# Performance work log

Hardware: AMD Instinct MI355X
Metric: run time of the kernel (lower is better)

## Reference

```python
import jax, jax.numpy as jnp
import numpy as np

UNITS = 128
INPUT_DIM = 784
OUTPUT_DIM = 10
NUM_LAYERS = 8
BATCH = 2048
DT = 0.1
EPS = 0.01
TOL = 1e-4
STEPS = 15


def setup_inputs() -> dict:
    key = jax.random.key(0)
    k = jax.random.split(key, 7)
    s_in = 1.0 / np.sqrt(INPUT_DIM)
    s_u = 1.0 / np.sqrt(UNITS)
    return {
        "x": jax.random.normal(k[0], (BATCH, INPUT_DIM), jnp.float32),
        "w_in": jax.random.uniform(k[1], (UNITS, INPUT_DIM), jnp.float32, -s_in, s_in),
        "b_in": jax.random.uniform(k[2], (UNITS,), jnp.float32, -s_in, s_in),
        "w_blocks": jax.random.uniform(k[3], (NUM_LAYERS, UNITS, UNITS), jnp.float32, -s_u, s_u),
        "b_blocks": jax.random.uniform(k[4], (NUM_LAYERS, UNITS), jnp.float32, -s_u, s_u),
        "w_out": jax.random.uniform(k[5], (OUTPUT_DIM, UNITS), jnp.float32, -s_u, s_u),
        "b_out": jax.random.uniform(k[6], (OUTPUT_DIM,), jnp.float32, -s_u, s_u),
    }


def _build_A(w_blocks):
    # A_l = [[I, dt*W_l], [-dt*W_l^T, (1+dt/eps)*I]], shape [L, 2u, 2u]
    I = jnp.broadcast_to(jnp.eye(UNITS, dtype=w_blocks.dtype), (NUM_LAYERS, UNITS, UNITS))
    top = jnp.concatenate([I, DT * w_blocks], axis=2)
    bot = jnp.concatenate([-DT * jnp.transpose(w_blocks, (0, 2, 1)), (1.0 + DT / EPS) * I], axis=2)
    return jnp.concatenate([top, bot], axis=1)


def _sweep(z_in, A, b_blocks):
    # Fixed-point sweeping (no-grad region in the original). z_ls: [L, B, 2u]
    B = z_in.shape[0]

    def layer_step(z, xs):
        A_l, b_l, z_l = xs
        rhs = jnp.concatenate(
            [jnp.broadcast_to(DT * b_l, (B, UNITS)), (DT / EPS) * jnp.tanh(z_l[:, :UNITS])],
            axis=1,
        ) + z
        # A_l is shared across the batch: one LU, many rhs
        y = jnp.linalg.solve(A_l, rhs.T).T
        err = jnp.mean(jnp.linalg.norm(z_l - y, axis=1))
        return y, (y, err)

    def body(state):
        z_ls, _, step = state
        _, (new_zls, errs) = jax.lax.scan(layer_step, z_in, (A, b_blocks, z_ls))
        return (new_zls, jnp.mean(errs), step + 1)

    def cond(state):
        _, err, step = state
        return jnp.logical_and(step < STEPS, err > TOL)

    z0 = jnp.broadcast_to(z_in[None], (NUM_LAYERS,) + z_in.shape)
    z_ls, _, _ = jax.lax.while_loop(cond, body, (z0, jnp.float32(10.0), jnp.int32(0)))
    return z_ls


def _block(z_in, W, b, z_l):
    # implicit_forward of one TransNetLayerSweeping (z_l is the converged sweep state)
    u_l, v_l = z_l[:, :UNITS], z_l[:, UNITS:]
    u_out = -DT * (v_l @ W.T) + z_in[:, :UNITS] + DT * b
    v_out = DT * (u_l @ W) + z_in[:, UNITS:] - (DT / EPS) * (v_l - jnp.tanh(u_l))
    return jnp.concatenate([u_out, v_out], axis=1)


def reference(x, w_in, b_in, w_blocks, b_blocks, w_out, b_out):
    x1 = x @ w_in.T + b_in                                  # [B, u]
    z_in = jnp.concatenate([x1, jnp.tanh(x1)], axis=1)      # [B, 2u]
    z_ls = _sweep(z_in, _build_A(w_blocks), b_blocks)       # [L, B, 2u]
    # Original loop does z = block.implicit_forward(z_in) for every block,
    # so only the LAST block's output survives.
    z_out = _block(z_in, w_blocks[-1], b_blocks[-1], z_ls[-1])
    logits = z_out[:, :UNITS] @ w_out.T + b_out             # [B, out]
    return jax.nn.softmax(logits, axis=1)
```

## Files before the change

### kernel.cpp

```cpp
#include <hip/hip_runtime.h>

#define U 128
#define BATCH 2048
#define NL 8
#define NS 8
#define DTc 0.1f
#define TENf 10.0f
#define INVC (1.0f/11.0f)
#define AFACT (0.01f/11.0f)
#define AST 264
#define HST 136

typedef unsigned short u16;
typedef unsigned int u32;
typedef __attribute__((ext_vector_type(8))) short bf16x8;
typedef __attribute__((ext_vector_type(4))) float f32x4;
#define MFMA16(a,b,c) __builtin_amdgcn_mfma_f32_16x16x32_bf16(a,b,c,0,0,0)

#define SWZ8(row, c8)  (((row)<<7) + ((((c8) ^ ((row)&7)))<<3))
#define SWZE(row, col) (SWZ8(row, (col)>>3) + ((col)&7))

__device__ __forceinline__ float bf2f(u16 h){ return __uint_as_float(((u32)h)<<16); }
__device__ __forceinline__ u16 f2bf(float f){
  u32 u = __float_as_uint(f);
  u += 0x7FFFu + ((u >> 16) & 1u);
  return (u16)(u >> 16);
}
__device__ __forceinline__ float fast_tanh(float x){
  float e = __expf(2.0f*x);
  return 1.0f - __fdividef(2.0f, e + 1.0f);
}
__device__ __forceinline__ int detect_md(const u16* x, int* s_bad, int t, int nthr){
  if(t==0) *s_bad = 0;
  __syncthreads();
  int f=0;
  for(int i=t;i<4096;i+=nthr){ float v = bf2f(x[i]); if(!(fabsf(v)<16.0f)) f=1; }
  if(f) atomicOr(s_bad,1);
  __syncthreads();
  return *s_bad ? 0 : 1;
}
__device__ __forceinline__ bf16x8 ld8f(const float* p){
  float4 f0 = *(const float4*)p, f1 = *(const float4*)(p+4);
  bf16x8 v;
  v[0]=(short)f2bf(f0.x); v[1]=(short)f2bf(f0.y); v[2]=(short)f2bf(f0.z); v[3]=(short)f2bf(f0.w);
  v[4]=(short)f2bf(f1.x); v[5]=(short)f2bf(f1.y); v[6]=(short)f2bf(f1.z); v[7]=(short)f2bf(f1.w);
  return v;
}
__device__ __forceinline__ void lgkm_barrier(){
  __builtin_amdgcn_sched_barrier(0);
  asm volatile("s_waitcnt lgkmcnt(0)\n\ts_barrier" ::: "memory");
  __builtin_amdgcn_sched_barrier(0);
}

template<typename GB, typename EPI>
__device__ __forceinline__ void gfull(const u16* __restrict__ A, GB getB, EPI epi,
                                      int w, int ln, int lq){
  const int n0 = 16*w + ln;
  bf16x8 bfr[4];
  #pragma unroll
  for(int kt=0;kt<4;kt++) bfr[kt] = getB(n0, kt*32 + lq*8);
  #pragma unroll 2
  for(int rt=0; rt<8; rt++){
    f32x4 acc = {0,0,0,0};
    #pragma unroll
    for(int kt=0;kt<4;kt++){
      bf16x8 af = *(const bf16x8*)&A[SWZ8(rt*16+ln, kt*4+lq)];
      acc = MFMA16(af, bfr[kt], acc);
    }
    epi(acc, rt*16 + lq*4, n0);
  }
}

__global__ __launch_bounds__(512) void prepB(
    const void* __restrict__ xraw, const void* __restrict__ wb,
    u16* __restrict__ Fsw, u16* __restrict__ Wfr){
  __shared__ u16 bufA[16384];
  __shared__ u16 bufB[16384];
  const int t = threadIdx.x;
  const int lane = t & 63, w = t >> 6, ln = lane & 15, lq = lane >> 4;
  const int L = blockIdx.x >> 3, mt = blockIdx.x & 7;
  const int md = detect_md((const u16*)xraw, (int*)bufA, t, 512);
  __syncthreads();
  const u16*   wbb = (const u16*)wb   + ((size_t)L<<14);
  const float* wbf = (const float*)wb + ((size_t)L<<14);

  if(t < 256){
    int kt = t >> 6, lanei = t & 63, lni = lanei & 15, lqi = lanei >> 4;
    bf16x8 v = md ? *(const bf16x8*)&wbb[(16*mt+lni)*U + 32*kt + 8*lqi]
                  : ld8f(wbf + (16*mt+lni)*U + 32*kt + 8*lqi);
    *(bf16x8*)&Wfr[((size_t)L*2048 + mt*256 + t)*8] = v;
  }

  for(int j8=t; j8<2048; j8+=512){
    int n = j8 >> 4, k0 = (j8 & 15) * 8;
    bf16x8 v = md ? *(const bf16x8*)&wbb[j8*8] : ld8f(wbf + j8*8);
    #pragma unroll
    for(int m=0;m<8;m++) bufA[SWZE(k0+m, n)] = (u16)v[m];
  }
  __syncthreads();

  auto gA = [&](int n,int k0)->bf16x8{ return *(const bf16x8*)&bufA[SWZ8(n, k0>>3)]; };
  auto gB = [&](int n,int k0)->bf16x8{ return *(const bf16x8*)&bufB[SWZ8(n, k0>>3)]; };
  auto gW = [&](int n,int k0)->bf16x8{
    if(md) return *(const bf16x8*)&wbb[n*U+k0];
    return ld8f(wbf + n*U + k0);
  };

  gfull(bufA, gA, [&](f32x4 acc, int rowb, int n0){
    #pragma unroll
    for(int r=0;r<4;r++) bufB[SWZE(rowb+r, n0)] = f2bf(AFACT*acc[r]);
  }, w, ln, lq);
  __syncthreads();
  gfull(bufB, gB, [&](f32x4 acc, int rowb, int n0){
    #pragma unroll
    for(int r=0;r<4;r++){
      int row = rowb + r;
      bufA[SWZE(row, n0)] = f2bf(INVC*(((row==n0)?1.0f:0.0f) - bf2f(bufB[SWZE(row, n0)]) + acc[r]));
    }
  }, w, ln, lq);
  __syncthreads();
  gfull(bufA, gW, [&](f32x4 acc, int rowb, int n0){
    #pragma unroll
    for(int r=0;r<4;r++) bufB[SWZE(rowb+r, n0)] = f2bf(DTc*acc[r]);
  }, w, ln, lq);
  __syncthreads();

  for(int i = mt*1024 + t; i < (mt+1)*1024; i += 512){
    int wf = (i>>11)&3;
    if(wf >= 2) continue;
    int lanei = i & 63, kt = (i>>6)&7, c = (i>>9)&3;
    int row_n = 64*wf + 16*c + (lanei & 15);
    int c8 = kt*4 + (lanei >> 4);
    bf16x8 v = (kt < 4) ? *(const bf16x8*)&bufA[SWZ8(row_n, c8)]
                        : *(const bf16x8*)&bufB[SWZ8(row_n, c8-16)];
    *(bf16x8*)&Fsw[((size_t)L*8192 + i)*8] = v;
  }
}

__global__ __launch_bounds__(512,2) void mainG(
    const void* __restrict__ xraw, const void* __restrict__ w_in,
    const void* __restrict__ b_in, const void* __restrict__ bb,
    const bf16x8* __restrict__ Fsw, const bf16x8* __restrict__ Wfr,
    const void* __restrict__ w_out, const void* __restrict__ b_out,
    void* __restrict__ outraw){
  __shared__ u16 At[2][16*AST];
  __shared__ u16 zh16[NL][16][132];
  __shared__ u16 Hld[16*HST];
  __shared__ float lg[16*12];
  __shared__ int s_bad;
  float* uout = (float*)&At[0][0];

  const int t = threadIdx.x;
  const int lane = t & 63, w = t >> 6, ln = lane & 15, lq = lane >> 4;
  const int r0 = blockIdx.x * 16;
  const int n = 16*w + ln;

  const int md = detect_md((const u16*)xraw, &s_bad, t, 512);
  float bbLr[NL];
  #pragma unroll
  for(int l=0;l<NL;l++)
    bbLr[l] = DTc * (md ? bf2f(((const u16*)bb)[l*U+n]) : ((const float*)bb)[l*U+n]);

  float zr[4];
  {
    const u16*   wrb = (const u16*)w_in   + (size_t)n*784;
    const float* wrf = (const float*)w_in + (size_t)n*784;
    const u16*   xrb = (const u16*)xraw   + (size_t)(r0+ln)*784;
    const float* xrf = (const float*)xraw + (size_t)(r0+ln)*784;
    f32x4 acc = {0,0,0,0};
    const bf16x8 z8 = {0,0,0,0,0,0,0,0};
    if(md){
      #pragma unroll
      for(int kt=0; kt<24; ++kt){
        int k0 = kt*32 + lq*8;
        acc = MFMA16(*(const bf16x8*)(xrb + k0), *(const bf16x8*)(wrb + k0), acc);
      }
      { int k0 = 768 + lq*8;
        bf16x8 av = z8, bv = z8;
        if(lq < 2){ av = *(const bf16x8*)(xrb + k0); bv = *(const bf16x8*)(wrb + k0); }
        acc = MFMA16(av, bv, acc);
      }
    } else {
      #pragma unroll 4
      for(int kt=0; kt<24; ++kt){
        int k0 = kt*32 + lq*8;
        acc = MFMA16(ld8f(xrf + k0), ld8f(wrf + k0), acc);
      }
      { int k0 = 768 + lq*8;
        bf16x8 av = z8, bv = z8;
        if(lq < 2){ av = ld8f(xrf + k0); bv = ld8f(wrf + k0); }
        acc = MFMA16(av, bv, acc);
      }
    }
    float bi = md ? bf2f(((const u16*)b_in)[n]) : ((const float*)b_in)[n];
    #pragma unroll
    for(int r=0;r<4;r++) zr[r] = acc[r] + bi;
  }

  #pragma unroll
  for(int l=0;l<NL;l++){
    #pragma unroll
    for(int r=0;r<4;r++) zh16[l][lq*4+r][n] = f2bf(zr[r]);
  }
  float ru[4];
  #pragma unroll
  for(int r=0;r<4;r++){
    int row = lq*4 + r;
    At[0][row*AST + n] = f2bf((TENf + 1.0f) * fast_tanh(zr[r]));
    float v = zr[r] + bbLr[0];
    ru[r] = v;
    At[0][row*AST + 128 + n] = f2bf(v);
  }
  const bf16x8* fbase = Fsw + (w>>2)*2048 + (w&3)*512 + lane;
  const bf16x8* wfb   = Wfr + w*256 + lane;
  bf16x8 BfA[8], BfB[8], WfA[4], WfB[4];
  #pragma unroll
  for(int kt=0;kt<8;kt++) BfA[kt] = fbase[kt*64];
  #pragma unroll
  for(int kt=0;kt<4;kt++) WfA[kt] = wfb[kt*64];
  __syncthreads();

#define STEPBODY(STEPV, BC, BN, WC, WN, CURC) { \
    const int l = (STEPV) & 7; \
    const int lnext = (l+1) & 7; \
    const bool last = ((STEPV) == NS*NL-1); \
    const bool wrap = (l == 7); \
    { const bf16x8* fp = fbase + lnext*8192; \
      _Pragma("unroll") \
      for(int kt=0;kt<8;kt++) BN[kt] = fp[kt*64]; \
      const bf16x8* wp = wfb + lnext*2048; \
      _Pragma("unroll") \
      for(int kt=0;kt<4;kt++) WN[kt] = wp[kt*64]; } \
    bf16x8 at8[8]; \
    _Pragma("unroll") \
    for(int kt=0;kt<8;kt++) at8[kt] = *(const bf16x8*)&At[CURC][ln*AST + kt*32 + lq*8]; \
    float th[4]; \
    if(!last){ \
      _Pragma("unroll") \
      for(int r=0;r<4;r++) th[r] = TENf * fast_tanh(bf2f(zh16[lnext][lq*4 + r][n])); \
    } \
    f32x4 accL = {0,0,0,0}; \
    _Pragma("unroll") \
    for(int kt=0;kt<8;kt++) accL = MFMA16(at8[kt], BC[kt], accL); \
    _Pragma("unroll") \
    for(int r=0;r<4;r++) Hld[(lq*4+r)*HST + n] = f2bf(accL[r]); \
    lgkm_barrier(); \
    bf16x8 hf[4]; \
    _Pragma("unroll") \
    for(int kt=0;kt<4;kt++) hf[kt] = *(const bf16x8*)&Hld[ln*HST + kt*32 + lq*8]; \
    f32x4 accR = {0,0,0,0}; \
    _Pragma("unroll") \
    for(int kt=0;kt<4;kt++) accR = MFMA16(hf[kt], WC[kt], accR); \
    if(!last){ \
      _Pragma("unroll") \
      for(int r=0;r<4;r++){ \
        int row = lq*4 + r; \
        float base = wrap ? fast_tanh(zr[r]) : accL[r]; \
        At[1-(CURC)][row*AST + n] = f2bf(th[r] + base); \
      } \
      _Pragma("unroll") \
      for(int r=0;r<4;r++){ \
        int row = lq*4 + r; \
        float yu = ru[r] - DTc*accR[r]; \
        zh16[l][row][n] = f2bf(yu); \
        float rn = wrap ? (zr[r] + bbLr[0]) : (yu + bbLr[(l+1)&7]); \
        ru[r] = rn; \
        At[1-(CURC)][row*AST + 128 + n] = f2bf(rn); \
      } \
    } else { \
      _Pragma("unroll") \
      for(int r=0;r<4;r++){ \
        int row = lq*4 + r; \
        uout[row*U + n] = zr[r] + bbLr[7] - DTc*accR[r]; \
      } \
    } \
    lgkm_barrier(); \
  }

  for(int sp=0; sp<NS*NL; sp+=2){
    STEPBODY(sp,   BfA, BfB, WfA, WfB, 0)
    STEPBODY(sp+1, BfB, BfA, WfB, WfA, 1)
  }
#undef STEPBODY

  if(t < 160){
    int mm = t/10, o = t - mm*10;
    float a = md ? bf2f(((const u16*)b_out)[o]) : ((const float*)b_out)[o];
    if(md){
      const u16* wo = (const u16*)w_out + o*U;
      for(int k=0;k<U;k++) a += uout[mm*U + k]*bf2f(wo[k]);
    } else {
      const float* wo = (const float*)w_out + o*U;
      for(int k=0;k<U;k++) a += uout[mm*U + k]*wo[k];
    }
    lg[mm*12 + o] = a;
  }
  __syncthreads();
  if(t < 16){
    float mx = -1e30f;
    for(int o=0;o<10;o++) mx = fmaxf(mx, lg[t*12 + o]);
    float e[10]; float sum = 0.0f;
    for(int o=0;o<10;o++){ e[o] = __expf(lg[t*12 + o] - mx); sum += e[o]; }
    float inv = 1.0f / sum;
    for(int o=0;o<10;o++){
      float pv = e[o]*inv;
      if(md) ((u16*)outraw)[(size_t)(r0 + t)*10 + o] = f2bf(pv);
      else   ((float*)outraw)[(size_t)(r0 + t)*10 + o] = pv;
    }
  }
}

extern "C" void kernel_launch(void* const* d_in, const int* in_sizes, int n_in,
                              void* d_out, int out_size, void* d_ws, size_t ws_size,
                              hipStream_t stream) {
  char* p = (char*)d_ws;
  u16* Fsw = (u16*)p;  p += (size_t)8*256*256*2;
  u16* Wfr = (u16*)p;  p += (size_t)8*128*128*2;

  prepB<<<64, 512, 0, stream>>>(d_in[0], d_in[3], Fsw, Wfr);
  mainG<<<BATCH/16, 512, 0, stream>>>(d_in[0], d_in[1], d_in[2], d_in[4],
                                      (const bf16x8*)Fsw, (const bf16x8*)Wfr,
                                      d_in[5], d_in[6], d_out);
}
```

Measured before the change: 187.6 us.

## Store MFMA operands in fragment order and keep sweep state in registers

The padded row-major LDS tiles for the A operand and the intermediate H are replaced with buffers laid out in MFMA fragment order, so each lane reads its 16-byte operand at lane*8 with no strided addressing. The per-layer sweep state zh16 moves out of LDS into a fully unrolled register array, which needs the layer loop to be unrolled 8 times so the indices are compile-time constants. The change is meant to cut LDS traffic, bank conflicts and address arithmetic in the latency-bound 64-step loop. In exchange it raises register pressure, which risks spills under the 512-thread, 2-block launch bound, and it grows code size.

```diff
diff --git a/kernel.cpp b/kernel.cpp
--- a/kernel.cpp
+++ b/kernel.cpp
@@ -8,8 +8,6 @@
 #define TENf 10.0f
 #define INVC (1.0f/11.0f)
 #define AFACT (0.01f/11.0f)
-#define AST 264
-#define HST 136
 
 typedef unsigned short u16;
 typedef unsigned int u32;
@@ -137,18 +135,17 @@
   }
 }
 
-__global__ __launch_bounds__(512,2) void mainG(
+__global__ __launch_bounds__(512,2) void mainH(
     const void* __restrict__ xraw, const void* __restrict__ w_in,
     const void* __restrict__ b_in, const void* __restrict__ bb,
     const bf16x8* __restrict__ Fsw, const bf16x8* __restrict__ Wfr,
     const void* __restrict__ w_out, const void* __restrict__ b_out,
     void* __restrict__ outraw){
-  __shared__ u16 At[2][16*AST];
-  __shared__ u16 zh16[NL][16][132];
-  __shared__ u16 Hld[16*HST];
+  __shared__ u16 Atf[2][4096];
+  __shared__ u16 Hf[2048];
   __shared__ float lg[16*12];
   __shared__ int s_bad;
-  float* uout = (float*)&At[0][0];
+  float* uout = (float*)&Atf[0][0];
 
   const int t = threadIdx.x;
   const int lane = t & 63, w = t >> 6, ln = lane & 15, lq = lane >> 4;
@@ -197,19 +194,22 @@
     for(int r=0;r<4;r++) zr[r] = acc[r] + bi;
   }
 
+  const int kT = n >> 5;
+  const int wbase = ((n>>3)&3)*128 + lq*32 + (n&7);
+
+  float zh[NL][4];
   #pragma unroll
   for(int l=0;l<NL;l++){
     #pragma unroll
-    for(int r=0;r<4;r++) zh16[l][lq*4+r][n] = f2bf(zr[r]);
+    for(int r=0;r<4;r++) zh[l][r] = bf2f(f2bf(zr[r]));
   }
   float ru[4];
   #pragma unroll
   for(int r=0;r<4;r++){
-    int row = lq*4 + r;
-    At[0][row*AST + n] = f2bf((TENf + 1.0f) * fast_tanh(zr[r]));
+    Atf[0][kT*512 + wbase + r*8] = f2bf((TENf + 1.0f) * fast_tanh(zr[r]));
     float v = zr[r] + bbLr[0];
     ru[r] = v;
-    At[0][row*AST + 128 + n] = f2bf(v);
+    Atf[0][(4+kT)*512 + wbase + r*8] = f2bf(v);
   }
   const bf16x8* fbase = Fsw + (w>>2)*2048 + (w&3)*512 + lane;
   const bf16x8* wfb   = Wfr + w*256 + lane;
@@ -220,68 +220,66 @@
   for(int kt=0;kt<4;kt++) WfA[kt] = wfb[kt*64];
   __syncthreads();
 
-#define STEPBODY(STEPV, BC, BN, WC, WN, CURC) { \
-    const int l = (STEPV) & 7; \
-    const int lnext = (l+1) & 7; \
-    const bool last = ((STEPV) == NS*NL-1); \
-    const bool wrap = (l == 7); \
-    { const bf16x8* fp = fbase + lnext*8192; \
+#define STEPB(L_, ITV, BC, BN, WC, WN, CURC) { \
+    const bool last = ((L_)==7) && ((ITV) == NS-1); \
+    { const bf16x8* fp = fbase + (((L_)+1)&7)*8192; \
       _Pragma("unroll") \
       for(int kt=0;kt<8;kt++) BN[kt] = fp[kt*64]; \
-      const bf16x8* wp = wfb + lnext*2048; \
+      const bf16x8* wp = wfb + (((L_)+1)&7)*2048; \
       _Pragma("unroll") \
       for(int kt=0;kt<4;kt++) WN[kt] = wp[kt*64]; } \
     bf16x8 at8[8]; \
     _Pragma("unroll") \
-    for(int kt=0;kt<8;kt++) at8[kt] = *(const bf16x8*)&At[CURC][ln*AST + kt*32 + lq*8]; \
+    for(int kt=0;kt<8;kt++) at8[kt] = *(const bf16x8*)&Atf[CURC][kt*512 + lane*8]; \
     float th[4]; \
     if(!last){ \
       _Pragma("unroll") \
-      for(int r=0;r<4;r++) th[r] = TENf * fast_tanh(bf2f(zh16[lnext][lq*4 + r][n])); \
+      for(int r=0;r<4;r++) th[r] = TENf * fast_tanh(zh[((L_)+1)&7][r]); \
     } \
     f32x4 accL = {0,0,0,0}; \
     _Pragma("unroll") \
     for(int kt=0;kt<8;kt++) accL = MFMA16(at8[kt], BC[kt], accL); \
     _Pragma("unroll") \
-    for(int r=0;r<4;r++) Hld[(lq*4+r)*HST + n] = f2bf(accL[r]); \
+    for(int r=0;r<4;r++) Hf[kT*512 + wbase + r*8] = f2bf(accL[r]); \
     lgkm_barrier(); \
     bf16x8 hf[4]; \
     _Pragma("unroll") \
-    for(int kt=0;kt<4;kt++) hf[kt] = *(const bf16x8*)&Hld[ln*HST + kt*32 + lq*8]; \
+    for(int kt=0;kt<4;kt++) hf[kt] = *(const bf16x8*)&Hf[kt*512 + lane*8]; \
     f32x4 accR = {0,0,0,0}; \
     _Pragma("unroll") \
     for(int kt=0;kt<4;kt++) accR = MFMA16(hf[kt], WC[kt], accR); \
     if(!last){ \
       _Pragma("unroll") \
       for(int r=0;r<4;r++){ \
-        int row = lq*4 + r; \
-        float base = wrap ? fast_tanh(zr[r]) : accL[r]; \
-        At[1-(CURC)][row*AST + n] = f2bf(th[r] + base); \
+        float base = ((L_)==7) ? fast_tanh(zr[r]) : accL[r]; \
+        Atf[1-(CURC)][kT*512 + wbase + r*8] = f2bf(th[r] + base); \
       } \
       _Pragma("unroll") \
       for(int r=0;r<4;r++){ \
-        int row = lq*4 + r; \
         float yu = ru[r] - DTc*accR[r]; \
-        zh16[l][row][n] = f2bf(yu); \
-        float rn = wrap ? (zr[r] + bbLr[0]) : (yu + bbLr[(l+1)&7]); \
+        zh[(L_)][r] = bf2f(f2bf(yu)); \
+        float rn = ((L_)==7) ? (zr[r] + bbLr[0]) : (yu + bbLr[((L_)+1)&7]); \
         ru[r] = rn; \
-        At[1-(CURC)][row*AST + 128 + n] = f2bf(rn); \
+        Atf[1-(CURC)][(4+kT)*512 + wbase + r*8] = f2bf(rn); \
       } \
     } else { \
       _Pragma("unroll") \
-      for(int r=0;r<4;r++){ \
-        int row = lq*4 + r; \
-        uout[row*U + n] = zr[r] + bbLr[7] - DTc*accR[r]; \
-      } \
+      for(int r=0;r<4;r++) uout[(lq*4+r)*U + n] = zr[r] + bbLr[7] - DTc*accR[r]; \
     } \
     lgkm_barrier(); \
   }
 
-  for(int sp=0; sp<NS*NL; sp+=2){
-    STEPBODY(sp,   BfA, BfB, WfA, WfB, 0)
-    STEPBODY(sp+1, BfB, BfA, WfB, WfA, 1)
-  }
-#undef STEPBODY
+  for(int it=0; it<NS; ++it){
+    STEPB(0, it, BfA, BfB, WfA, WfB, 0)
+    STEPB(1, it, BfB, BfA, WfB, WfA, 1)
+    STEPB(2, it, BfA, BfB, WfA, WfB, 0)
+    STEPB(3, it, BfB, BfA, WfB, WfA, 1)
+    STEPB(4, it, BfA, BfB, WfA, WfB, 0)
+    STEPB(5, it, BfB, BfA, WfB, WfA, 1)
+    STEPB(6, it, BfA, BfB, WfA, WfB, 0)
+    STEPB(7, it, BfB, BfA, WfB, WfA, 1)
+  }
+#undef STEPB
 
   if(t < 160){
     int mm = t/10, o = t - mm*10;
@@ -318,7 +316,7 @@
   u16* Wfr = (u16*)p;  p += (size_t)8*128*128*2;
 
   prepB<<<64, 512, 0, stream>>>(d_in[0], d_in[3], Fsw, Wfr);
-  mainG<<<BATCH/16, 512, 0, stream>>>(d_in[0], d_in[1], d_in[2], d_in[4],
+  mainH<<<BATCH/16, 512, 0, stream>>>(d_in[0], d_in[1], d_in[2], d_in[4],
                                       (const bf16x8*)Fsw, (const bf16x8*)Wfr,
                                       d_in[5], d_in[6], d_out);
 }
```

Measured after the change: 344.0 us. 1.83x slower.
